# Kernel optimization log

Measured on AMD Instinct MI355X. Metric: run time of the kernel, lower is better.

## Reference

```python
import jax, jax.numpy as jnp
import numpy as np

B, Q, L = 64, 64, 8192
KC = 51            # NarrowConv1D kernel size
HC = KC // 2 + 1   # 26 raw symmetric-half params
N = 500
KT = N + 1         # 501 transpose-conv kernel size
HT = KT // 2 + 1   # 251 raw half params

@jax.custom_vjp
def sigmoid_st(u):
    # Sigmoid forward, straight-through (identity) backward
    return jax.nn.sigmoid(u)

def _sst_fwd(u):
    return jax.nn.sigmoid(u), None

def _sst_bwd(res, g):
    return (g,)

sigmoid_st.defvjp(_sst_fwd, _sst_bwd)

def symmetric(w):
    # cat(X, X[..., :-1].flip(-1)) -> symmetric kernel of odd length
    return jnp.concatenate([w, w[..., :-1][..., ::-1]], axis=-1)

def depthwise_conv(x, k, pad):
    # x: [B, Q, L]; k: [Q, K] one kernel per channel (groups == channels)
    return jax.lax.conv_general_dilated(
        x, k[:, None, :], window_strides=(1,), padding=[(pad, pad)],
        dimension_numbers=("NCH", "OIH", "NCH"), feature_group_count=x.shape[1])

def setup_inputs() -> dict:
    key = jax.random.key(0)
    k1, k2, k3, k4 = jax.random.split(key, 4)
    return {
        "x": jax.random.normal(k1, (B, Q, L), dtype=jnp.float32),
        "conv_w_half": jax.random.normal(k2, (HC,), dtype=jnp.float32) * 0.1,
        "tc_w_half": jax.random.normal(k3, (Q, HT), dtype=jnp.float32),
        "A_raw": jax.random.normal(k4, (Q,), dtype=jnp.float32),
    }

def reference(x, conv_w_half, tc_w_half, A_raw):
    # 1) NarrowConv1D: one symmetric kernel shared across all Q channels
    kc = symmetric(conv_w_half)                       # [51]
    kc_full = jnp.broadcast_to(kc, (Q, KC))           # ChannelSame expand
    x = depthwise_conv(x, kc_full, KC // 2)           # [B,Q,L], 'same'

    # 2) softmax over spectral axis
    x = jax.nn.softmax(x, axis=-1)

    # 3) SymmetricNormConvTranspose1d: sigmoid(straight-through) + symmetric;
    #    stride-1 transpose conv with symmetric kernel == depthwise conv with
    #    padding K-1-p = N//2
    wt = sigmoid_st(tc_w_half)                        # [Q, 251] in (0,1)
    kt = symmetric(wt)                                # [Q, 501]
    x = depthwise_conv(x, kt, N // 2)                 # [B,Q,L]

    # 4) serial lattice (reflection/transmission) recursion over Q channels
    a = sigmoid_st(A_raw)                             # [Q]
    xs = jnp.transpose(x, (1, 0, 2))                  # [Q,B,L]

    def step(carry, inp):
        r, t2 = carry
        rn, aq = inp
        tn = 1.0 - rn
        s = 1.0 / (1.0 - aq * r * rn)
        r_new = r + aq * rn * t2 * s
        t2_new = aq * t2 * tn * tn * s * s
        return (r_new, t2_new), None

    init = (jnp.zeros_like(xs[0]), jnp.ones_like(xs[0]))
    (r, _), _ = jax.lax.scan(step, init, (xs, a))

    peak = wt[-1, -1]                                 # weight[-1,0,N//2] (kernel center)
    r = r / (peak * jnp.prod(a))
    return r                                          # [B, L]
```

## Files before the change

kernel.cpp:

```cpp
#include <hip/hip_runtime.h>

#define B_ 64
#define Q_ 64
#define L_ 8192
#define KCONV 51
#define HC 26
#define HT 251
#define NCH2 34
#define NCH1 6

#define A51_OFF 512
#define TA_OFF  8192
#define RN_OFF  2236416

#define MAPB(s) ((((s) & ~7) | ((((s) & 7) + ((s) >> 3)) & 7)) << 4)

typedef _Float16 f16x8 __attribute__((ext_vector_type(8)));
typedef float f32x16 __attribute__((ext_vector_type(16)));
typedef unsigned int uix2 __attribute__((ext_vector_type(2)));

__device__ __forceinline__ float sigm(float v) {
    return 1.0f / (1.0f + __expf(-v));
}

__global__ __launch_bounds__(256) void k_params(const float* __restrict__ cwh,
                                                const float* __restrict__ tcw,
                                                const float* __restrict__ araw,
                                                float* __restrict__ ws) {
    const int tid = threadIdx.x;
    const int q = blockIdx.x;
    char* wsb = (char*)ws;
    if (q < Q_) {
        for (int idx = tid; idx < NCH2 * 64; idx += 256) {
            int c = idx >> 6, lane = idx & 63;
            int hi = lane >> 5, i = lane & 31;
            int mbase = 16 * c + 8 * hi - i - 6;
            f16x8 hv;
            #pragma unroll
            for (int jj = 0; jj < 8; jj++) {
                int m = mbase + jj;
                float v = 0.0f;
                if (m >= 0 && m <= 500) {
                    int hh = (m <= 250) ? m : (500 - m);
                    v = sigm(tcw[q * HT + hh]);
                }
                hv[jj] = (_Float16)v;
            }
            *(f16x8*)(wsb + TA_OFF + ((size_t)q * (NCH2 * 64) + idx) * 16) = hv;
        }
    } else {
        if (tid < Q_) ws[tid] = sigm(araw[tid]);
        for (int idx = tid; idx < NCH1 * 64; idx += 256) {
            int c = idx >> 6, lane = idx & 63;
            int hi = lane >> 5, i = lane & 31;
            int mbase = 16 * c + 8 * hi - i - 7;
            f16x8 hv;
            #pragma unroll
            for (int jj = 0; jj < 8; jj++) {
                int m = mbase + jj;
                float v = 0.0f;
                if (m >= 0 && m < KCONV) v = cwh[m < HC ? m : (KCONV - 1 - m)];
                hv[jj] = (_Float16)v;
            }
            *(f16x8*)(wsb + A51_OFF + idx * 16) = hv;
        }
        __syncthreads();
        if (tid == 0) {
            float p = 1.0f;
            for (int j = 0; j < Q_; j++) p *= ws[j];
            float peak = sigm(tcw[(Q_ - 1) * HT + 250]);
            ws[64] = 1.0f / (peak * p);
        }
    }
}

__device__ __forceinline__ void write_dlayout(char* buf, int base_slot,
                                              const float* v, float scale,
                                              int w, int j, int hi) {
    union P4 { _Float16 h[4]; uint2 u; };
    P4 p[4];
    #pragma unroll
    for (int k = 0; k < 4; k++) {
        #pragma unroll
        for (int d = 0; d < 4; d++) p[k].h[d] = (_Float16)(v[4 * k + d] * scale);
    }
#if __has_builtin(__builtin_amdgcn_permlane32_swap)
    uix2 s0x = __builtin_amdgcn_permlane32_swap(p[0].u.x, p[2].u.x, false, false);
    uix2 s0y = __builtin_amdgcn_permlane32_swap(p[0].u.y, p[2].u.y, false, false);
    uix2 s1x = __builtin_amdgcn_permlane32_swap(p[1].u.x, p[3].u.x, false, false);
    uix2 s1y = __builtin_amdgcn_permlane32_swap(p[1].u.y, p[3].u.y, false, false);
    uint4 w0, w1;
    if (hi == 0) {
        w0.x = p[0].u.x; w0.y = p[0].u.y; w0.z = s0x[1]; w0.w = s0y[1];
        w1.x = p[1].u.x; w1.y = p[1].u.y; w1.z = s1x[1]; w1.w = s1y[1];
    } else {
        w0.x = s0x[0]; w0.y = s0y[0]; w0.z = p[2].u.x; w0.w = p[2].u.y;
        w1.x = s1x[0]; w1.y = s1y[0]; w1.z = p[3].u.x; w1.w = p[3].u.y;
    }
    const int s0 = base_slot + 128 * w + 4 * j + 2 * hi;
    *(uint4*)(buf + MAPB(s0)) = w0;
    *(uint4*)(buf + MAPB(s0 + 1)) = w1;
#else
    #pragma unroll
    for (int k = 0; k < 4; k++) {
        const int bo = MAPB(base_slot + 128 * w + 4 * j + k) + 8 * hi;
        *(uint2*)(buf + bo) = p[k].u;
    }
#endif
}

__global__ __launch_bounds__(512, 4) void k_fused(const float* __restrict__ x,
                                                  float* __restrict__ ws) {
    const int tid = threadIdx.x;
    const int bid = blockIdx.x;
    const int q = bid >> 5, pr = bid & 31;
    const int row0 = (2 * pr) * Q_ + q, row1 = (2 * pr + 1) * Q_ + q;
    char* wsb = (char*)ws;
    __shared__ __attribute__((aligned(128))) char bufA[17408];
    __shared__ __attribute__((aligned(128))) char bufB[17408];
    __shared__ float red[32];

    const int w = tid >> 6, lane = tid & 63, j = lane & 31, hi = lane >> 5;

    f16x8 a51r[NCH1];
    #pragma unroll
    for (int c = 0; c < NCH1; c++)
        a51r[c] = *(const f16x8*)(wsb + A51_OFF + (c * 64 + lane) * 16);

    const uint4 z4 = {0u, 0u, 0u, 0u};
    if (tid < 32) {
        *(uint4*)(bufA + MAPB(tid)) = z4;
        *(uint4*)(bufB + MAPB(tid)) = z4;
    } else if (tid >= 64 && tid < 96) {
        int s = 1056 + (tid - 64);
        *(uint4*)(bufA + MAPB(s)) = z4;
        *(uint4*)(bufB + MAPB(s)) = z4;
    }

    union H8 { _Float16 h[8]; uint4 u; };
    {
        #pragma unroll
        for (int r = 0; r < 2; r++) {
            const float* xr = x + (size_t)(r ? row1 : row0) * L_ + 16 * tid;
            char* buf = r ? bufB : bufA;
            float4 f0 = *(const float4*)(xr + 0);
            float4 f1 = *(const float4*)(xr + 4);
            float4 f2 = *(const float4*)(xr + 8);
            float4 f3 = *(const float4*)(xr + 12);
            H8 h0, h1;
            h0.h[0] = (_Float16)f0.x; h0.h[1] = (_Float16)f0.y;
            h0.h[2] = (_Float16)f0.z; h0.h[3] = (_Float16)f0.w;
            h0.h[4] = (_Float16)f1.x; h0.h[5] = (_Float16)f1.y;
            h0.h[6] = (_Float16)f1.z; h0.h[7] = (_Float16)f1.w;
            h1.h[0] = (_Float16)f2.x; h1.h[1] = (_Float16)f2.y;
            h1.h[2] = (_Float16)f2.z; h1.h[3] = (_Float16)f2.w;
            h1.h[4] = (_Float16)f3.x; h1.h[5] = (_Float16)f3.y;
            h1.h[6] = (_Float16)f3.z; h1.h[7] = (_Float16)f3.w;
            *(uint4*)(buf + MAPB(2 * tid + 32)) = h0.u;
            *(uint4*)(buf + MAPB(2 * tid + 33)) = h1.u;
        }
    }
    __syncthreads();

    f32x16 acc0 = {}, acc1 = {};
    {
        f16x8 pA[2], pB[2];
        pA[0] = *(const f16x8*)(bufA + MAPB(128 * w + 4 * j + 28 + hi));
        pB[0] = *(const f16x8*)(bufB + MAPB(128 * w + 4 * j + 28 + hi));
        pA[1] = *(const f16x8*)(bufA + MAPB(128 * w + 4 * j + 30 + hi));
        pB[1] = *(const f16x8*)(bufB + MAPB(128 * w + 4 * j + 30 + hi));
        #pragma unroll
        for (int c = 0; c < NCH1; c++) {
            acc0 = __builtin_amdgcn_mfma_f32_32x32x16_f16(a51r[c], pA[c & 1], acc0, 0, 0, 0);
            acc1 = __builtin_amdgcn_mfma_f32_32x32x16_f16(a51r[c], pB[c & 1], acc1, 0, 0, 0);
            if (c + 2 < NCH1) {
                const int bo = MAPB(128 * w + 4 * j + 2 * (c + 2) + 28 + hi);
                pA[c & 1] = *(const f16x8*)(bufA + bo);
                pB[c & 1] = *(const f16x8*)(bufB + bo);
            }
        }
    }

    float mx0 = -3.402823466e+38f, mx1 = -3.402823466e+38f;
    #pragma unroll
    for (int e = 0; e < 16; e++) { mx0 = fmaxf(mx0, acc0[e]); mx1 = fmaxf(mx1, acc1[e]); }
    #pragma unroll
    for (int o = 32; o > 0; o >>= 1) {
        mx0 = fmaxf(mx0, __shfl_xor(mx0, o));
        mx1 = fmaxf(mx1, __shfl_xor(mx1, o));
    }
    float sm0 = 0.0f, sm1 = 0.0f;
    #pragma unroll
    for (int e = 0; e < 16; e++) {
        acc0[e] = __expf(acc0[e] - mx0); sm0 += acc0[e];
        acc1[e] = __expf(acc1[e] - mx1); sm1 += acc1[e];
    }
    #pragma unroll
    for (int o = 32; o > 0; o >>= 1) { sm0 += __shfl_xor(sm0, o); sm1 += __shfl_xor(sm1, o); }
    if (lane == 0) {
        red[w] = mx0; red[8 + w] = sm0;
        red[16 + w] = mx1; red[24 + w] = sm1;
    }
    __syncthreads();
    float mg0 = red[0], mg1 = red[16];
    #pragma unroll
    for (int i = 1; i < 8; i++) { mg0 = fmaxf(mg0, red[i]); mg1 = fmaxf(mg1, red[16 + i]); }
    float ss0 = 0.0f, ss1 = 0.0f;
    #pragma unroll
    for (int i = 0; i < 8; i++) {
        ss0 += red[8 + i] * __expf(red[i] - mg0);
        ss1 += red[24 + i] * __expf(red[16 + i] - mg1);
    }
    const float isum0 = __expf(mx0 - mg0) / ss0;
    const float isum1 = __expf(mx1 - mg1) / ss1;

    write_dlayout(bufA, 32, (const float*)&acc0, isum0, w, j, hi);
    write_dlayout(bufB, 32, (const float*)&acc1, isum1, w, j, hi);
    __syncthreads();

    const char* tab6 = wsb + TA_OFF + ((size_t)q * (NCH2 * 64) + lane) * 16;
    f32x16 o0 = {}, o1 = {};
    {
        f16x8 afr[8], pA[2], pB[2];
        #pragma unroll
        for (int c = 0; c < 8; c++)
            afr[c] = *(const f16x8*)(tab6 + c * 1024);
        #pragma unroll
        for (int c = 0; c < 2; c++) {
            const int bo = MAPB(128 * w + 4 * j + 2 * c + hi);
            pA[c] = *(const f16x8*)(bufA + bo);
            pB[c] = *(const f16x8*)(bufB + bo);
        }
        #pragma unroll
        for (int c = 0; c < NCH2; c++) {
            o0 = __builtin_amdgcn_mfma_f32_32x32x16_f16(afr[c & 7], pA[c & 1], o0, 0, 0, 0);
            o1 = __builtin_amdgcn_mfma_f32_32x32x16_f16(afr[c & 7], pB[c & 1], o1, 0, 0, 0);
            if (c + 2 < NCH2) {
                const int bo = MAPB(128 * w + 4 * j + 2 * (c + 2) + hi);
                pA[c & 1] = *(const f16x8*)(bufA + bo);
                pB[c & 1] = *(const f16x8*)(bufB + bo);
            }
            if (c + 8 < NCH2)
                afr[c & 7] = *(const f16x8*)(tab6 + (c + 8) * 1024);
        }
    }
    __syncthreads();

    write_dlayout(bufA, 0, (const float*)&o0, 1.0f, w, j, hi);
    write_dlayout(bufB, 0, (const float*)&o1, 1.0f, w, j, hi);
    __syncthreads();
    {
        uint4 r0 = *(uint4*)(bufA + MAPB(2 * tid));
        uint4 r1 = *(uint4*)(bufA + MAPB(2 * tid + 1));
        char* dst = wsb + RN_OFF + ((size_t)row0 * L_ + 16 * tid) * 2;
        *(uint4*)dst = r0;
        *(uint4*)(dst + 16) = r1;
        uint4 r2 = *(uint4*)(bufB + MAPB(2 * tid));
        uint4 r3 = *(uint4*)(bufB + MAPB(2 * tid + 1));
        char* dst1 = wsb + RN_OFF + ((size_t)row1 * L_ + 16 * tid) * 2;
        *(uint4*)dst1 = r2;
        *(uint4*)(dst1 + 16) = r3;
    }
}

__global__ __launch_bounds__(256) void k_lat(const float* __restrict__ ws,
                                             float* __restrict__ out) {
    const int tid = threadIdx.x;
    const int T = blockIdx.x & 7, b = blockIdx.x >> 3;
    const char* wsb = (const char*)ws;
    const int l = 1024 * T + 4 * tid;
    const char* src = wsb + RN_OFF + ((size_t)(b * Q_) * L_ + l) * 2;
    float r[4] = {0.0f, 0.0f, 0.0f, 0.0f};
    float t2[4] = {1.0f, 1.0f, 1.0f, 1.0f};
    union P4 { _Float16 h[4]; uint2 u; };
    P4 cur;
    cur.u = *(const uint2*)src;
    for (int q = 0; q < Q_; q++) {
        P4 nxt = cur;
        if (q < Q_ - 1) nxt.u = *(const uint2*)(src + (size_t)(q + 1) * L_ * 2);
        const float aq = ws[q];
        #pragma unroll
        for (int e = 0; e < 4; e++) {
            float rn = (float)cur.h[e], tn = 1.0f - rn;
            float si = 1.0f / (1.0f - aq * r[e] * rn);
            float rnew = r[e] + aq * rn * t2[e] * si;
            t2[e] = aq * t2[e] * tn * tn * si * si;
            r[e] = rnew;
        }
        cur = nxt;
    }
    const float inv_scale = ws[64];
    float4 o;
    o.x = r[0] * inv_scale; o.y = r[1] * inv_scale;
    o.z = r[2] * inv_scale; o.w = r[3] * inv_scale;
    *(float4*)&out[(size_t)b * L_ + l] = o;
}

extern "C" void kernel_launch(void* const* d_in, const int* in_sizes, int n_in,
                              void* d_out, int out_size, void* d_ws, size_t ws_size,
                              hipStream_t stream) {
    (void)in_sizes; (void)n_in; (void)out_size; (void)ws_size;
    const float* x    = (const float*)d_in[0];
    const float* cwh  = (const float*)d_in[1];
    const float* tcw  = (const float*)d_in[2];
    const float* araw = (const float*)d_in[3];
    float* out = (float*)d_out;
    float* ws  = (float*)d_ws;

    hipLaunchKernelGGL(k_params, dim3(Q_ + 1), dim3(256), 0, stream, cwh, tcw, araw, ws);
    hipLaunchKernelGGL(k_fused, dim3((B_ / 2) * Q_), dim3(512), 0, stream, x, ws);
    hipLaunchKernelGGL(k_lat, dim3(B_ * 8), dim3(256), 0, stream, ws, out);
}
```

Before: 101.8 us.

## Process four batch rows per block in fused conv-softmax-conv kernel

Each block now handles four rows of the same channel instead of two, so every MFMA A-operand fragment (conv weights and the per-channel transpose-conv table) is reused across four accumulators. The grid is halved, and the A51 fragments are reloaded from global memory per chunk rather than held in registers. The goal is to amortize weight loads and raise MFMA density per wave. The cost is about 70KB of LDS per block and more accumulator registers, which limits occupancy and reduces the number of blocks available to fill the GPU.

Result: slower. 108.3 us (+6.4%).

```diff
diff --git a/kernel.cpp b/kernel.cpp
--- a/kernel.cpp
+++ b/kernel.cpp
@@ -113,153 +113,152 @@
                                                   float* __restrict__ ws) {
     const int tid = threadIdx.x;
     const int bid = blockIdx.x;
-    const int q = bid >> 5, pr = bid & 31;
-    const int row0 = (2 * pr) * Q_ + q, row1 = (2 * pr + 1) * Q_ + q;
+    const int q = bid >> 4, qd = bid & 15;
     char* wsb = (char*)ws;
-    __shared__ __attribute__((aligned(128))) char bufA[17408];
-    __shared__ __attribute__((aligned(128))) char bufB[17408];
-    __shared__ float red[32];
+    __shared__ __attribute__((aligned(128))) char buf[4][17408];
+    __shared__ float red[64];
 
     const int w = tid >> 6, lane = tid & 63, j = lane & 31, hi = lane >> 5;
-
-    f16x8 a51r[NCH1];
-    #pragma unroll
-    for (int c = 0; c < NCH1; c++)
-        a51r[c] = *(const f16x8*)(wsb + A51_OFF + (c * 64 + lane) * 16);
+    int rows[4];
+    #pragma unroll
+    for (int r = 0; r < 4; r++) rows[r] = (4 * qd + r) * Q_ + q;
 
     const uint4 z4 = {0u, 0u, 0u, 0u};
     if (tid < 32) {
-        *(uint4*)(bufA + MAPB(tid)) = z4;
-        *(uint4*)(bufB + MAPB(tid)) = z4;
+        #pragma unroll
+        for (int r = 0; r < 4; r++) *(uint4*)(buf[r] + MAPB(tid)) = z4;
     } else if (tid >= 64 && tid < 96) {
         int s = 1056 + (tid - 64);
-        *(uint4*)(bufA + MAPB(s)) = z4;
-        *(uint4*)(bufB + MAPB(s)) = z4;
+        #pragma unroll
+        for (int r = 0; r < 4; r++) *(uint4*)(buf[r] + MAPB(s)) = z4;
     }
 
     union H8 { _Float16 h[8]; uint4 u; };
+    #pragma unroll
+    for (int r = 0; r < 4; r++) {
+        const float* xr = x + (size_t)rows[r] * L_ + 16 * tid;
+        float4 f0 = *(const float4*)(xr + 0);
+        float4 f1 = *(const float4*)(xr + 4);
+        float4 f2 = *(const float4*)(xr + 8);
+        float4 f3 = *(const float4*)(xr + 12);
+        H8 h0, h1;
+        h0.h[0] = (_Float16)f0.x; h0.h[1] = (_Float16)f0.y;
+        h0.h[2] = (_Float16)f0.z; h0.h[3] = (_Float16)f0.w;
+        h0.h[4] = (_Float16)f1.x; h0.h[5] = (_Float16)f1.y;
+        h0.h[6] = (_Float16)f1.z; h0.h[7] = (_Float16)f1.w;
+        h1.h[0] = (_Float16)f2.x; h1.h[1] = (_Float16)f2.y;
+        h1.h[2] = (_Float16)f2.z; h1.h[3] = (_Float16)f2.w;
+        h1.h[4] = (_Float16)f3.x; h1.h[5] = (_Float16)f3.y;
+        h1.h[6] = (_Float16)f3.z; h1.h[7] = (_Float16)f3.w;
+        *(uint4*)(buf[r] + MAPB(2 * tid + 32)) = h0.u;
+        *(uint4*)(buf[r] + MAPB(2 * tid + 33)) = h1.u;
+    }
+    __syncthreads();
+
+    f32x16 acc[4] = {};
     {
-        #pragma unroll
-        for (int r = 0; r < 2; r++) {
-            const float* xr = x + (size_t)(r ? row1 : row0) * L_ + 16 * tid;
-            char* buf = r ? bufB : bufA;
-            float4 f0 = *(const float4*)(xr + 0);
-            float4 f1 = *(const float4*)(xr + 4);
-            float4 f2 = *(const float4*)(xr + 8);
-            float4 f3 = *(const float4*)(xr + 12);
-            H8 h0, h1;
-            h0.h[0] = (_Float16)f0.x; h0.h[1] = (_Float16)f0.y;
-            h0.h[2] = (_Float16)f0.z; h0.h[3] = (_Float16)f0.w;
-            h0.h[4] = (_Float16)f1.x; h0.h[5] = (_Float16)f1.y;
-            h0.h[6] = (_Float16)f1.z; h0.h[7] = (_Float16)f1.w;
-            h1.h[0] = (_Float16)f2.x; h1.h[1] = (_Float16)f2.y;
-            h1.h[2] = (_Float16)f2.z; h1.h[3] = (_Float16)f2.w;
-            h1.h[4] = (_Float16)f3.x; h1.h[5] = (_Float16)f3.y;
-            h1.h[6] = (_Float16)f3.z; h1.h[7] = (_Float16)f3.w;
-            *(uint4*)(buf + MAPB(2 * tid + 32)) = h0.u;
-            *(uint4*)(buf + MAPB(2 * tid + 33)) = h1.u;
-        }
-    }
-    __syncthreads();
-
-    f32x16 acc0 = {}, acc1 = {};
-    {
-        f16x8 pA[2], pB[2];
-        pA[0] = *(const f16x8*)(bufA + MAPB(128 * w + 4 * j + 28 + hi));
-        pB[0] = *(const f16x8*)(bufB + MAPB(128 * w + 4 * j + 28 + hi));
-        pA[1] = *(const f16x8*)(bufA + MAPB(128 * w + 4 * j + 30 + hi));
-        pB[1] = *(const f16x8*)(bufB + MAPB(128 * w + 4 * j + 30 + hi));
+        f16x8 p[4][2];
+        #pragma unroll
+        for (int r = 0; r < 4; r++) {
+            p[r][0] = *(const f16x8*)(buf[r] + MAPB(128 * w + 4 * j + 28 + hi));
+            p[r][1] = *(const f16x8*)(buf[r] + MAPB(128 * w + 4 * j + 30 + hi));
+        }
         #pragma unroll
         for (int c = 0; c < NCH1; c++) {
-            acc0 = __builtin_amdgcn_mfma_f32_32x32x16_f16(a51r[c], pA[c & 1], acc0, 0, 0, 0);
-            acc1 = __builtin_amdgcn_mfma_f32_32x32x16_f16(a51r[c], pB[c & 1], acc1, 0, 0, 0);
+            f16x8 a51 = *(const f16x8*)(wsb + A51_OFF + (c * 64 + lane) * 16);
+            #pragma unroll
+            for (int r = 0; r < 4; r++)
+                acc[r] = __builtin_amdgcn_mfma_f32_32x32x16_f16(a51, p[r][c & 1], acc[r], 0, 0, 0);
             if (c + 2 < NCH1) {
                 const int bo = MAPB(128 * w + 4 * j + 2 * (c + 2) + 28 + hi);
-                pA[c & 1] = *(const f16x8*)(bufA + bo);
-                pB[c & 1] = *(const f16x8*)(bufB + bo);
+                #pragma unroll
+                for (int r = 0; r < 4; r++)
+                    p[r][c & 1] = *(const f16x8*)(buf[r] + bo);
             }
         }
     }
 
-    float mx0 = -3.402823466e+38f, mx1 = -3.402823466e+38f;
-    #pragma unroll
-    for (int e = 0; e < 16; e++) { mx0 = fmaxf(mx0, acc0[e]); mx1 = fmaxf(mx1, acc1[e]); }
-    #pragma unroll
-    for (int o = 32; o > 0; o >>= 1) {
-        mx0 = fmaxf(mx0, __shfl_xor(mx0, o));
-        mx1 = fmaxf(mx1, __shfl_xor(mx1, o));
-    }
-    float sm0 = 0.0f, sm1 = 0.0f;
-    #pragma unroll
-    for (int e = 0; e < 16; e++) {
-        acc0[e] = __expf(acc0[e] - mx0); sm0 += acc0[e];
-        acc1[e] = __expf(acc1[e] - mx1); sm1 += acc1[e];
-    }
-    #pragma unroll
-    for (int o = 32; o > 0; o >>= 1) { sm0 += __shfl_xor(sm0, o); sm1 += __shfl_xor(sm1, o); }
+    float mxr[4], smr[4];
+    #pragma unroll
+    for (int r = 0; r < 4; r++) {
+        float mx = -3.402823466e+38f;
+        #pragma unroll
+        for (int e = 0; e < 16; e++) mx = fmaxf(mx, acc[r][e]);
+        #pragma unroll
+        for (int o = 32; o > 0; o >>= 1) mx = fmaxf(mx, __shfl_xor(mx, o));
+        float sm = 0.0f;
+        #pragma unroll
+        for (int e = 0; e < 16; e++) { acc[r][e] = __expf(acc[r][e] - mx); sm += acc[r][e]; }
+        #pragma unroll
+        for (int o = 32; o > 0; o >>= 1) sm += __shfl_xor(sm, o);
+        mxr[r] = mx; smr[r] = sm;
+    }
     if (lane == 0) {
-        red[w] = mx0; red[8 + w] = sm0;
-        red[16 + w] = mx1; red[24 + w] = sm1;
-    }
-    __syncthreads();
-    float mg0 = red[0], mg1 = red[16];
-    #pragma unroll
-    for (int i = 1; i < 8; i++) { mg0 = fmaxf(mg0, red[i]); mg1 = fmaxf(mg1, red[16 + i]); }
-    float ss0 = 0.0f, ss1 = 0.0f;
-    #pragma unroll
-    for (int i = 0; i < 8; i++) {
-        ss0 += red[8 + i] * __expf(red[i] - mg0);
-        ss1 += red[24 + i] * __expf(red[16 + i] - mg1);
-    }
-    const float isum0 = __expf(mx0 - mg0) / ss0;
-    const float isum1 = __expf(mx1 - mg1) / ss1;
-
-    write_dlayout(bufA, 32, (const float*)&acc0, isum0, w, j, hi);
-    write_dlayout(bufB, 32, (const float*)&acc1, isum1, w, j, hi);
+        #pragma unroll
+        for (int r = 0; r < 4; r++) {
+            red[r * 16 + w] = mxr[r];
+            red[r * 16 + 8 + w] = smr[r];
+        }
+    }
+    __syncthreads();
+    float isum[4];
+    #pragma unroll
+    for (int r = 0; r < 4; r++) {
+        float mg = red[r * 16];
+        #pragma unroll
+        for (int i = 1; i < 8; i++) mg = fmaxf(mg, red[r * 16 + i]);
+        float ss = 0.0f;
+        #pragma unroll
+        for (int i = 0; i < 8; i++) ss += red[r * 16 + 8 + i] * __expf(red[r * 16 + i] - mg);
+        isum[r] = __expf(mxr[r] - mg) / ss;
+    }
+
+    #pragma unroll
+    for (int r = 0; r < 4; r++)
+        write_dlayout(buf[r], 32, (const float*)&acc[r], isum[r], w, j, hi);
     __syncthreads();
 
     const char* tab6 = wsb + TA_OFF + ((size_t)q * (NCH2 * 64) + lane) * 16;
-    f32x16 o0 = {}, o1 = {};
+    f32x16 o[4] = {};
     {
-        f16x8 afr[8], pA[2], pB[2];
-        #pragma unroll
-        for (int c = 0; c < 8; c++)
+        f16x8 afr[4], pb[4][2];
+        #pragma unroll
+        for (int c = 0; c < 4; c++)
             afr[c] = *(const f16x8*)(tab6 + c * 1024);
         #pragma unroll
-        for (int c = 0; c < 2; c++) {
-            const int bo = MAPB(128 * w + 4 * j + 2 * c + hi);
-            pA[c] = *(const f16x8*)(bufA + bo);
-            pB[c] = *(const f16x8*)(bufB + bo);
+        for (int r = 0; r < 4; r++) {
+            #pragma unroll
+            for (int c = 0; c < 2; c++)
+                pb[r][c] = *(const f16x8*)(buf[r] + MAPB(128 * w + 4 * j + 2 * c + hi));
         }
         #pragma unroll
         for (int c = 0; c < NCH2; c++) {
-            o0 = __builtin_amdgcn_mfma_f32_32x32x16_f16(afr[c & 7], pA[c & 1], o0, 0, 0, 0);
-            o1 = __builtin_amdgcn_mfma_f32_32x32x16_f16(afr[c & 7], pB[c & 1], o1, 0, 0, 0);
+            #pragma unroll
+            for (int r = 0; r < 4; r++)
+                o[r] = __builtin_amdgcn_mfma_f32_32x32x16_f16(afr[c & 3], pb[r][c & 1], o[r], 0, 0, 0);
             if (c + 2 < NCH2) {
                 const int bo = MAPB(128 * w + 4 * j + 2 * (c + 2) + hi);
-                pA[c & 1] = *(const f16x8*)(bufA + bo);
-                pB[c & 1] = *(const f16x8*)(bufB + bo);
+                #pragma unroll
+                for (int r = 0; r < 4; r++)
+                    pb[r][c & 1] = *(const f16x8*)(buf[r] + bo);
             }
-            if (c + 8 < NCH2)
-                afr[c & 7] = *(const f16x8*)(tab6 + (c + 8) * 1024);
-        }
-    }
-    __syncthreads();
-
-    write_dlayout(bufA, 0, (const float*)&o0, 1.0f, w, j, hi);
-    write_dlayout(bufB, 0, (const float*)&o1, 1.0f, w, j, hi);
-    __syncthreads();
-    {
-        uint4 r0 = *(uint4*)(bufA + MAPB(2 * tid));
-        uint4 r1 = *(uint4*)(bufA + MAPB(2 * tid + 1));
-        char* dst = wsb + RN_OFF + ((size_t)row0 * L_ + 16 * tid) * 2;
+            if (c + 4 < NCH2)
+                afr[c & 3] = *(const f16x8*)(tab6 + (c + 4) * 1024);
+        }
+    }
+    __syncthreads();
+
+    #pragma unroll
+    for (int r = 0; r < 4; r++)
+        write_dlayout(buf[r], 0, (const float*)&o[r], 1.0f, w, j, hi);
+    __syncthreads();
+    #pragma unroll
+    for (int r = 0; r < 4; r++) {
+        uint4 r0 = *(uint4*)(buf[r] + MAPB(2 * tid));
+        uint4 r1 = *(uint4*)(buf[r] + MAPB(2 * tid + 1));
+        char* dst = wsb + RN_OFF + ((size_t)rows[r] * L_ + 16 * tid) * 2;
         *(uint4*)dst = r0;
         *(uint4*)(dst + 16) = r1;
-        uint4 r2 = *(uint4*)(bufB + MAPB(2 * tid));
-        uint4 r3 = *(uint4*)(bufB + MAPB(2 * tid + 1));
-        char* dst1 = wsb + RN_OFF + ((size_t)row1 * L_ + 16 * tid) * 2;
-        *(uint4*)dst1 = r2;
-        *(uint4*)(dst1 + 16) = r3;
     }
 }
 
@@ -308,6 +307,6 @@
     float* ws  = (float*)d_ws;
 
     hipLaunchKernelGGL(k_params, dim3(Q_ + 1), dim3(256), 0, stream, cwh, tcw, araw, ws);
-    hipLaunchKernelGGL(k_fused, dim3((B_ / 2) * Q_), dim3(512), 0, stream, x, ws);
+    hipLaunchKernelGGL(k_fused, dim3((B_ / 4) * Q_), dim3(512), 0, stream, x, ws);
     hipLaunchKernelGGL(k_lat, dim3(B_ * 8), dim3(256), 0, stream, ws, out);
 }
```
